# Optimization experiments

Hardware: AMD Instinct MI355X
Metric: run time of the kernel (lower is better)

The kernel has to match this reference:

```python
import jax, jax.numpy as jnp
import numpy as np

B, H, Wd, C = 8, 64, 64, 128
KH, KW = 3, 3
N = KH * KW  # kernel_n
F = 256


def _grid_offset(h, w, kh, kw):
    """Replicates the TensorLayer grid construction exactly, including the
    (2,kh,kw)->(kh*kw,2) reshape of the stacked meshgrid."""
    n = kh * kw
    initial = np.stack(np.meshgrid(np.arange(kh), np.arange(kw), indexing='ij'))  # (2,kh,kw)
    initial = initial.reshape(-1, 2).astype(np.float32)  # (n,2), faithful flattening order
    gy = np.arange(-int((kh - 1) / 2.0), h - int((kh - 1) / 2.0))
    gx = np.arange(-int((kw - 1) / 2.0), w - int((kw - 1) / 2.0))
    grid = np.stack(np.meshgrid(gy, gx, indexing='ij'), axis=-1).astype(np.float32)  # (h,w,2)
    grid = np.tile(grid[:, :, None, :], (1, 1, n, 1))  # (h,w,n,2)
    return jnp.asarray(grid + initial[None, None, :, :])  # (h,w,n,2)


def setup_inputs() -> dict:
    key = jax.random.key(0)
    k1, k2, k3 = jax.random.split(key, 3)
    x = jax.random.normal(k1, (B, H, Wd, C), dtype=jnp.float32)
    offsets = jax.random.normal(k2, (B, H, Wd, 2 * N), dtype=jnp.float32)
    W = jax.random.normal(k3, (N, C, F), dtype=jnp.float32) * 0.02  # truncated_normal(0.02) analogue
    b = jnp.zeros((F,), dtype=jnp.float32)
    return {"x": x, "offsets": offsets, "W": W, "b": b}


def reference(x, offsets, W, b):
    h, w = x.shape[1], x.shape[2]
    grid = _grid_offset(h, w, KH, KW)  # (h,w,n,2)
    coords = grid[None] + offsets.reshape(x.shape[0], h, w, N, 2)  # (b,h,w,n,2)
    cy = jnp.clip(coords[..., 0], 0.0, jnp.float32(h - 1))
    cx = jnp.clip(coords[..., 1], 0.0, jnp.float32(w - 1))
    y0 = jnp.floor(cy).astype(jnp.int32)
    y1 = jnp.ceil(cy).astype(jnp.int32)
    x0 = jnp.floor(cx).astype(jnp.int32)
    x1 = jnp.ceil(cx).astype(jnp.int32)

    bidx = jnp.arange(x.shape[0])[:, None, None, None]

    def gather(yy, xx):
        return x[bidx, yy, xx]  # (b,h,w,n,c)

    v_lt = gather(y0, x0)
    v_rb = gather(y1, x1)
    v_lb = gather(y0, x1)  # (lt_y, rb_x) as in original
    v_rt = gather(y1, x0)  # (rb_y, lt_x) as in original

    fy = (cy - y0.astype(cy.dtype))[..., None]
    fx = (cx - x0.astype(cx.dtype))[..., None]
    vals_t = v_lt + (v_rt - v_lt) * fy
    vals_b = v_lb + (v_rb - v_lb) * fy
    mapped = vals_t + (vals_b - vals_t) * fx  # (b,h,w,n,c)

    # conv3d with kernel [1,1,n,c,f] + VALID == contraction over (n,c)
    out = jnp.einsum('bhwnc,ncf->bhwf', mapped, W) + b
    return out
```

## Files before the change

kernel.cpp:

```cpp
#include <hip/hip_runtime.h>

#define HH 64
#define WW 64
#define CC 128
#define FF 256
#define NTAP 9
#define KD 1152
#define XELEMS (8 * HH * WW * CC)
#define XCVT_BLOCKS (XELEMS / (256 * 8))
#define WT_BLOCKS 144

typedef __attribute__((ext_vector_type(8))) short bf16x8;
typedef __attribute__((ext_vector_type(4))) float floatx4;

__device__ inline unsigned short f2bf(float v) {
  union { float f; unsigned u; } c; c.f = v;
  unsigned r = (c.u + 0x7FFFu + ((c.u >> 16) & 1u)) >> 16;
  return (unsigned short)r;
}
__device__ inline float bflo(unsigned u) {
  union { unsigned u; float f; } c; c.u = u << 16; return c.f;
}
__device__ inline float bfhi(unsigned u) {
  union { unsigned u; float f; } c; c.u = u & 0xFFFF0000u; return c.f;
}

__device__ inline unsigned lerp_word(unsigned u00, unsigned u10, unsigned u01, unsigned u11,
                                     float fy, float fx) {
  float v00 = bflo(u00), v10 = bflo(u10), v01 = bflo(u01), v11 = bflo(u11);
  float tx = v00 + (v10 - v00) * fy;
  float tb = v01 + (v11 - v01) * fy;
  unsigned short rlo = f2bf(tx + (tb - tx) * fx);
  v00 = bfhi(u00); v10 = bfhi(u10); v01 = bfhi(u01); v11 = bfhi(u11);
  tx = v00 + (v10 - v00) * fy;
  tb = v01 + (v11 - v01) * fy;
  unsigned short rhi = f2bf(tx + (tb - tx) * fx);
  return (unsigned)rlo | ((unsigned)rhi << 16);
}

#define IY_PACK 0x18690
#define IX_PACK 0x21894

struct ITap { int b00, b10, b01, b11; float fy, fx; };

__device__ inline ITap interp_setup(const float* __restrict__ offp, int i, int p, int nx) {
  const int n = nx >> 1;
  const float2 o2 = *(const float2*)(offp + 2 * n);
  float cy = (float)(i - 1 + ((IY_PACK >> (2 * n)) & 3)) + o2.x;
  float cx = (float)(p - 1 + ((IX_PACK >> (2 * n)) & 3)) + o2.y;
  cy = fminf(fmaxf(cy, 0.f), 63.f);
  cx = fminf(fmaxf(cx, 0.f), 63.f);
  const float fy0 = floorf(cy), fx0 = floorf(cx);
  const int y0 = (int)fy0, y1 = (int)ceilf(cy);
  const int x0 = (int)fx0, x1 = (int)ceilf(cx);
  ITap t;
  t.b00 = (y0 * WW + x0) * CC;
  t.b10 = (y1 * WW + x0) * CC;
  t.b01 = (y0 * WW + x1) * CC;
  t.b11 = (y1 * WW + x1) * CC;
  t.fy = cy - fy0;
  t.fx = cx - fx0;
  return t;
}

__global__ void prep_kernel(const float* __restrict__ X, const float* __restrict__ W,
                            unsigned short* __restrict__ Xb, unsigned short* __restrict__ Wt) {
  const int blk = blockIdx.x;
  if (blk < XCVT_BLOCKS) {
    const int t = blk * 256 + threadIdx.x;
    const float4* src = (const float4*)(X + (size_t)t * 8);
    float4 a = src[0], b2 = src[1];
    bf16x8 o;
    o[0] = (short)f2bf(a.x);  o[1] = (short)f2bf(a.y);
    o[2] = (short)f2bf(a.z);  o[3] = (short)f2bf(a.w);
    o[4] = (short)f2bf(b2.x); o[5] = (short)f2bf(b2.y);
    o[6] = (short)f2bf(b2.z); o[7] = (short)f2bf(b2.w);
    *(bf16x8*)(Xb + (size_t)t * 8) = o;
  } else {
    const int t = (blk - XCVT_BLOCKS) * 256 + threadIdx.x;
    const int f = t & 255;
    const int k0 = (t >> 8) * 8;
    unsigned short o[8];
#pragma unroll
    for (int i2 = 0; i2 < 8; ++i2)
      o[i2] = f2bf(W[(size_t)(k0 + i2) * FF + f]);
    *(uint4*)(Wt + (size_t)f * KD + k0) = *(uint4*)o;
  }
}

__global__ __launch_bounds__(256, 2) void fused_kernel(
    const unsigned short* __restrict__ Xb, const float* __restrict__ Off,
    const unsigned short* __restrict__ Wt, const float* __restrict__ bias,
    float* __restrict__ Out)
{
  __shared__ unsigned short smA[64 * 64];
  __shared__ unsigned short smB[256 * 64];

  const int blk = blockIdx.x;
  const int b   = blk & 7;
  const int i   = blk >> 3;
  const int m0  = (b * 64 + i) * 64;
  const int tid = threadIdx.x;
  const int wave = tid >> 6, lane = tid & 63;
  const int wf   = wave * 64;
  const int arow = lane & 15, aq = lane >> 4;
  const int srow = tid >> 3, sch = tid & 7;
  const int p = tid >> 2, c0 = tid & 3;

  const unsigned short* xb = Xb + (size_t)b * (HH * WW * CC);
  const float* offp = Off + ((size_t)(b * HH + i) * WW + p) * (2 * NTAP);

  floatx4 acc[4][4];
#pragma unroll
  for (int mt = 0; mt < 4; ++mt)
#pragma unroll
    for (int ft = 0; ft < 4; ++ft)
      acc[mt][ft] = (floatx4){0.f, 0.f, 0.f, 0.f};

#define STAGE_B(KT)                                                                  \
  {                                                                                  \
    _Pragma("unroll")                                                                \
    for (int q2 = 0; q2 < 8; ++q2) {                                                 \
      const int row = q2 * 32 + srow;                                                \
      const int chp = sch ^ (row & 7);                                               \
      const unsigned short* gp = Wt + (size_t)row * KD + (KT) * 64 + chp * 8;        \
      unsigned short* l = (unsigned short*)&smB[row * 64 + sch * 8];                 \
      __builtin_amdgcn_global_load_lds(                                              \
          (const __attribute__((address_space(1))) unsigned int*)gp,                 \
          (__attribute__((address_space(3))) unsigned int*)l, 16, 0, 0);             \
    }                                                                                \
  }

  {
    ITap t = interp_setup(offp, i, p, 0);
#pragma unroll
    for (int cc = 0; cc < 2; ++cc) {
      const int c = c0 + cc * 4;
      const int ch = c << 3;
      uint4 q00 = *(const uint4*)(xb + t.b00 + ch);
      uint4 q10 = *(const uint4*)(xb + t.b10 + ch);
      uint4 q01 = *(const uint4*)(xb + t.b01 + ch);
      uint4 q11 = *(const uint4*)(xb + t.b11 + ch);
      unsigned ow0 = lerp_word(q00.x, q10.x, q01.x, q11.x, t.fy, t.fx);
      unsigned ow1 = lerp_word(q00.y, q10.y, q01.y, q11.y, t.fy, t.fx);
      unsigned ow2 = lerp_word(q00.z, q10.z, q01.z, q11.z, t.fy, t.fx);
      unsigned ow3 = lerp_word(q00.w, q10.w, q01.w, q11.w, t.fy, t.fx);
      *(uint4*)&smA[p * 64 + ((c ^ (p & 7)) << 3)] = make_uint4(ow0, ow1, ow2, ow3);
    }
    STAGE_B(0)
  }
  __syncthreads();

  for (int kt = 0; kt < 18; ++kt) {
    bf16x8 afr[2][4], bfr[2][4];
#pragma unroll
    for (int ks = 0; ks < 2; ++ks) {
      const int slot = (((ks * 4 + aq) ^ (arow & 7)) << 3);
#pragma unroll
      for (int mt = 0; mt < 4; ++mt)
        afr[ks][mt] = *(const bf16x8*)&smA[(mt * 16 + arow) * 64 + slot];
#pragma unroll
      for (int ft = 0; ft < 4; ++ft)
        bfr[ks][ft] = *(const bf16x8*)&smB[(wf + ft * 16 + arow) * 64 + slot];
    }
    __syncthreads();

    const int nx = kt + 1;
    ITap t;
    uint4 g[2][4];
    if (nx < 18) {
      t = interp_setup(offp, i, p, nx);
      const int gc = (nx & 1) << 3;
#pragma unroll
      for (int cc = 0; cc < 2; ++cc) {
        const int ch = (gc + c0 + cc * 4) << 3;
        g[cc][0] = *(const uint4*)(xb + t.b00 + ch);
        g[cc][1] = *(const uint4*)(xb + t.b10 + ch);
        g[cc][2] = *(const uint4*)(xb + t.b01 + ch);
        g[cc][3] = *(const uint4*)(xb + t.b11 + ch);
      }
      STAGE_B(nx)
    }

#pragma unroll
    for (int ks = 0; ks < 2; ++ks)
#pragma unroll
      for (int mt = 0; mt < 4; ++mt)
#pragma unroll
        for (int ft = 0; ft < 4; ++ft)
          acc[mt][ft] = __builtin_amdgcn_mfma_f32_16x16x32_bf16(
              afr[ks][mt], bfr[ks][ft], acc[mt][ft], 0, 0, 0);

    if (nx < 18) {
#pragma unroll
      for (int cc = 0; cc < 2; ++cc) {
        const int c = c0 + cc * 4;
        uint4 q00 = g[cc][0], q10 = g[cc][1], q01 = g[cc][2], q11 = g[cc][3];
        unsigned ow0 = lerp_word(q00.x, q10.x, q01.x, q11.x, t.fy, t.fx);
        unsigned ow1 = lerp_word(q00.y, q10.y, q01.y, q11.y, t.fy, t.fx);
        unsigned ow2 = lerp_word(q00.z, q10.z, q01.z, q11.z, t.fy, t.fx);
        unsigned ow3 = lerp_word(q00.w, q10.w, q01.w, q11.w, t.fy, t.fx);
        *(uint4*)&smA[p * 64 + ((c ^ (p & 7)) << 3)] = make_uint4(ow0, ow1, ow2, ow3);
      }
    }
    __syncthreads();
  }
#undef STAGE_B

  float bv[4];
#pragma unroll
  for (int ft = 0; ft < 4; ++ft)
    bv[ft] = bias[wf + ft * 16 + arow];
#pragma unroll
  for (int mt = 0; mt < 4; ++mt) {
#pragma unroll
    for (int ft = 0; ft < 4; ++ft) {
      const int f = wf + ft * 16 + arow;
#pragma unroll
      for (int r = 0; r < 4; ++r) {
        const int m = m0 + mt * 16 + aq * 4 + r;
        Out[(size_t)m * FF + f] = acc[mt][ft][r] + bv[ft];
      }
    }
  }
}

extern "C" void kernel_launch(void* const* d_in, const int* in_sizes, int n_in,
                              void* d_out, int out_size, void* d_ws, size_t ws_size,
                              hipStream_t stream) {
  const float* X    = (const float*)d_in[0];
  const float* Off  = (const float*)d_in[1];
  const float* W    = (const float*)d_in[2];
  const float* bias = (const float*)d_in[3];
  float* Out = (float*)d_out;

  unsigned short* Wt = (unsigned short*)d_ws;
  unsigned short* Xb = Wt + (size_t)FF * KD;

  prep_kernel<<<XCVT_BLOCKS + WT_BLOCKS, 256, 0, stream>>>(X, W, Xb, Wt);
  fused_kernel<<<512, 256, 0, stream>>>(Xb, Off, Wt, bias, Out);
}
```

Baseline: 120.1 us.

## Use 512-thread blocks with 2x4 wave tiling and packed bf16 conversion

Doubles the fused kernel's block size to 8 waves, each computing a 32x64 output tile instead of 64x64. Each thread now gathers and interpolates one 8-channel chunk rather than two, and B staging is split across more threads. The intent is more latency hiding for the bilinear gathers and lower register pressure per thread. Separately, the manual float-to-bf16 rounding is replaced with the hardware v_cvt_pk_bf16_f32 instruction, which cuts ALU work in the lerp; in exchange each B fragment is now read from LDS by two waves.

```diff
diff --git a/kernel.cpp b/kernel.cpp
--- a/kernel.cpp
+++ b/kernel.cpp
@@ -24,18 +24,23 @@
 __device__ inline float bfhi(unsigned u) {
   union { unsigned u; float f; } c; c.u = u & 0xFFFF0000u; return c.f;
 }
+__device__ inline unsigned cvt_pk_bf16(float lo, float hi) {
+  unsigned r;
+  asm("v_cvt_pk_bf16_f32 %0, %1, %2" : "=v"(r) : "v"(lo), "v"(hi));
+  return r;
+}
 
 __device__ inline unsigned lerp_word(unsigned u00, unsigned u10, unsigned u01, unsigned u11,
                                      float fy, float fx) {
   float v00 = bflo(u00), v10 = bflo(u10), v01 = bflo(u01), v11 = bflo(u11);
   float tx = v00 + (v10 - v00) * fy;
   float tb = v01 + (v11 - v01) * fy;
-  unsigned short rlo = f2bf(tx + (tb - tx) * fx);
+  float rlo = tx + (tb - tx) * fx;
   v00 = bfhi(u00); v10 = bfhi(u10); v01 = bfhi(u01); v11 = bfhi(u11);
   tx = v00 + (v10 - v00) * fy;
   tb = v01 + (v11 - v01) * fy;
-  unsigned short rhi = f2bf(tx + (tb - tx) * fx);
-  return (unsigned)rlo | ((unsigned)rhi << 16);
+  float rhi = tx + (tb - tx) * fx;
+  return cvt_pk_bf16(rlo, rhi);
 }
 
 #define IY_PACK 0x18690
@@ -88,7 +93,7 @@
   }
 }
 
-__global__ __launch_bounds__(256, 2) void fused_kernel(
+__global__ __launch_bounds__(512, 4) void fused_kernel(
     const unsigned short* __restrict__ Xb, const float* __restrict__ Off,
     const unsigned short* __restrict__ Wt, const float* __restrict__ bias,
     float* __restrict__ Out)
@@ -102,17 +107,18 @@
   const int m0  = (b * 64 + i) * 64;
   const int tid = threadIdx.x;
   const int wave = tid >> 6, lane = tid & 63;
-  const int wf   = wave * 64;
+  const int wm   = (wave & 1) * 32;
+  const int wf   = (wave >> 1) * 64;
   const int arow = lane & 15, aq = lane >> 4;
-  const int srow = tid >> 3, sch = tid & 7;
-  const int p = tid >> 2, c0 = tid & 3;
+  const int p  = tid >> 3;
+  const int c0 = tid & 7;
 
   const unsigned short* xb = Xb + (size_t)b * (HH * WW * CC);
-  const float* offp = Off + ((size_t)(b * HH + i) * WW + p) * (2 * NTAP);
-
-  floatx4 acc[4][4];
-#pragma unroll
-  for (int mt = 0; mt < 4; ++mt)
+  const float* offp = Off + ((size_t)(b * 64 + i) * 64 + p) * (2 * NTAP);
+
+  floatx4 acc[2][4];
+#pragma unroll
+  for (int mt = 0; mt < 2; ++mt)
 #pragma unroll
     for (int ft = 0; ft < 4; ++ft)
       acc[mt][ft] = (floatx4){0.f, 0.f, 0.f, 0.f};
@@ -120,11 +126,11 @@
 #define STAGE_B(KT)                                                                  \
   {                                                                                  \
     _Pragma("unroll")                                                                \
-    for (int q2 = 0; q2 < 8; ++q2) {                                                 \
-      const int row = q2 * 32 + srow;                                                \
-      const int chp = sch ^ (row & 7);                                               \
+    for (int q2 = 0; q2 < 4; ++q2) {                                                 \
+      const int row = q2 * 64 + (tid >> 3);                                          \
+      const int chp = c0 ^ (row & 7);                                                \
       const unsigned short* gp = Wt + (size_t)row * KD + (KT) * 64 + chp * 8;        \
-      unsigned short* l = (unsigned short*)&smB[row * 64 + sch * 8];                 \
+      unsigned short* l = (unsigned short*)&smB[row * 64 + c0 * 8];                  \
       __builtin_amdgcn_global_load_lds(                                              \
           (const __attribute__((address_space(1))) unsigned int*)gp,                 \
           (__attribute__((address_space(3))) unsigned int*)l, 16, 0, 0);             \
@@ -133,32 +139,28 @@
 
   {
     ITap t = interp_setup(offp, i, p, 0);
-#pragma unroll
-    for (int cc = 0; cc < 2; ++cc) {
-      const int c = c0 + cc * 4;
-      const int ch = c << 3;
-      uint4 q00 = *(const uint4*)(xb + t.b00 + ch);
-      uint4 q10 = *(const uint4*)(xb + t.b10 + ch);
-      uint4 q01 = *(const uint4*)(xb + t.b01 + ch);
-      uint4 q11 = *(const uint4*)(xb + t.b11 + ch);
-      unsigned ow0 = lerp_word(q00.x, q10.x, q01.x, q11.x, t.fy, t.fx);
-      unsigned ow1 = lerp_word(q00.y, q10.y, q01.y, q11.y, t.fy, t.fx);
-      unsigned ow2 = lerp_word(q00.z, q10.z, q01.z, q11.z, t.fy, t.fx);
-      unsigned ow3 = lerp_word(q00.w, q10.w, q01.w, q11.w, t.fy, t.fx);
-      *(uint4*)&smA[p * 64 + ((c ^ (p & 7)) << 3)] = make_uint4(ow0, ow1, ow2, ow3);
-    }
+    const int ch = c0 * 8;
+    uint4 q00 = *(const uint4*)(xb + t.b00 + ch);
+    uint4 q10 = *(const uint4*)(xb + t.b10 + ch);
+    uint4 q01 = *(const uint4*)(xb + t.b01 + ch);
+    uint4 q11 = *(const uint4*)(xb + t.b11 + ch);
+    unsigned ow0 = lerp_word(q00.x, q10.x, q01.x, q11.x, t.fy, t.fx);
+    unsigned ow1 = lerp_word(q00.y, q10.y, q01.y, q11.y, t.fy, t.fx);
+    unsigned ow2 = lerp_word(q00.z, q10.z, q01.z, q11.z, t.fy, t.fx);
+    unsigned ow3 = lerp_word(q00.w, q10.w, q01.w, q11.w, t.fy, t.fx);
+    *(uint4*)&smA[p * 64 + ((c0 ^ (p & 7)) << 3)] = make_uint4(ow0, ow1, ow2, ow3);
     STAGE_B(0)
   }
   __syncthreads();
 
   for (int kt = 0; kt < 18; ++kt) {
-    bf16x8 afr[2][4], bfr[2][4];
+    bf16x8 afr[2][2], bfr[2][4];
 #pragma unroll
     for (int ks = 0; ks < 2; ++ks) {
       const int slot = (((ks * 4 + aq) ^ (arow & 7)) << 3);
 #pragma unroll
-      for (int mt = 0; mt < 4; ++mt)
-        afr[ks][mt] = *(const bf16x8*)&smA[(mt * 16 + arow) * 64 + slot];
+      for (int mt = 0; mt < 2; ++mt)
+        afr[ks][mt] = *(const bf16x8*)&smA[(wm + mt * 16 + arow) * 64 + slot];
 #pragma unroll
       for (int ft = 0; ft < 4; ++ft)
         bfr[ks][ft] = *(const bf16x8*)&smB[(wf + ft * 16 + arow) * 64 + slot];
@@ -167,41 +169,32 @@
 
     const int nx = kt + 1;
     ITap t;
-    uint4 g[2][4];
+    uint4 g00, g10, g01, g11;
     if (nx < 18) {
       t = interp_setup(offp, i, p, nx);
-      const int gc = (nx & 1) << 3;
-#pragma unroll
-      for (int cc = 0; cc < 2; ++cc) {
-        const int ch = (gc + c0 + cc * 4) << 3;
-        g[cc][0] = *(const uint4*)(xb + t.b00 + ch);
-        g[cc][1] = *(const uint4*)(xb + t.b10 + ch);
-        g[cc][2] = *(const uint4*)(xb + t.b01 + ch);
-        g[cc][3] = *(const uint4*)(xb + t.b11 + ch);
-      }
+      const int ch = ((nx & 1) * 8 + c0) * 8;
+      g00 = *(const uint4*)(xb + t.b00 + ch);
+      g10 = *(const uint4*)(xb + t.b10 + ch);
+      g01 = *(const uint4*)(xb + t.b01 + ch);
+      g11 = *(const uint4*)(xb + t.b11 + ch);
       STAGE_B(nx)
     }
 
 #pragma unroll
     for (int ks = 0; ks < 2; ++ks)
 #pragma unroll
-      for (int mt = 0; mt < 4; ++mt)
+      for (int mt = 0; mt < 2; ++mt)
 #pragma unroll
         for (int ft = 0; ft < 4; ++ft)
           acc[mt][ft] = __builtin_amdgcn_mfma_f32_16x16x32_bf16(
               afr[ks][mt], bfr[ks][ft], acc[mt][ft], 0, 0, 0);
 
     if (nx < 18) {
-#pragma unroll
-      for (int cc = 0; cc < 2; ++cc) {
-        const int c = c0 + cc * 4;
-        uint4 q00 = g[cc][0], q10 = g[cc][1], q01 = g[cc][2], q11 = g[cc][3];
-        unsigned ow0 = lerp_word(q00.x, q10.x, q01.x, q11.x, t.fy, t.fx);
-        unsigned ow1 = lerp_word(q00.y, q10.y, q01.y, q11.y, t.fy, t.fx);
-        unsigned ow2 = lerp_word(q00.z, q10.z, q01.z, q11.z, t.fy, t.fx);
-        unsigned ow3 = lerp_word(q00.w, q10.w, q01.w, q11.w, t.fy, t.fx);
-        *(uint4*)&smA[p * 64 + ((c ^ (p & 7)) << 3)] = make_uint4(ow0, ow1, ow2, ow3);
-      }
+      unsigned ow0 = lerp_word(g00.x, g10.x, g01.x, g11.x, t.fy, t.fx);
+      unsigned ow1 = lerp_word(g00.y, g10.y, g01.y, g11.y, t.fy, t.fx);
+      unsigned ow2 = lerp_word(g00.z, g10.z, g01.z, g11.z, t.fy, t.fx);
+      unsigned ow3 = lerp_word(g00.w, g10.w, g01.w, g11.w, t.fy, t.fx);
+      *(uint4*)&smA[p * 64 + ((c0 ^ (p & 7)) << 3)] = make_uint4(ow0, ow1, ow2, ow3);
     }
     __syncthreads();
   }
@@ -212,13 +205,13 @@
   for (int ft = 0; ft < 4; ++ft)
     bv[ft] = bias[wf + ft * 16 + arow];
 #pragma unroll
-  for (int mt = 0; mt < 4; ++mt) {
+  for (int mt = 0; mt < 2; ++mt) {
 #pragma unroll
     for (int ft = 0; ft < 4; ++ft) {
       const int f = wf + ft * 16 + arow;
 #pragma unroll
       for (int r = 0; r < 4; ++r) {
-        const int m = m0 + mt * 16 + aq * 4 + r;
+        const int m = m0 + wm + mt * 16 + aq * 4 + r;
         Out[(size_t)m * FF + f] = acc[mt][ft][r] + bv[ft];
       }
     }
@@ -238,5 +231,5 @@
   unsigned short* Xb = Wt + (size_t)FF * KD;
 
   prep_kernel<<<XCVT_BLOCKS + WT_BLOCKS, 256, 0, stream>>>(X, W, Xb, Wt);
-  fused_kernel<<<512, 256, 0, stream>>>(Xb, Off, Wt, bias, Out);
-}
+  fused_kernel<<<512, 512, 0, stream>>>(Xb, Off, Wt, bias, Out);
+}
```

New measurement: 112.6 us. 1.07x faster.

## Gather fp32 X directly, widen K-tile to a full tap, split-K across waves

Applied to the files above, without the earlier changes.

Drops the separate X-to-bf16 conversion pass, so the fused kernel gathers fp32 X and packs to bf16 with v_cvt_pk_bf16_f32. The K tile grows to one full tap (128 channels), halving the loop trip count. Block size goes to 512 threads, with two wave groups splitting K and reducing through shared memory before the store. This removes one full read/write pass over X and some barriers. In exchange the gather reads twice as many bytes, the prefetch/compute overlap is dropped, and shared memory grows to about 80KB per block.

```diff
diff --git a/kernel.cpp b/kernel.cpp
--- a/kernel.cpp
+++ b/kernel.cpp
@@ -6,8 +6,6 @@
 #define FF 256
 #define NTAP 9
 #define KD 1152
-#define XELEMS (8 * HH * WW * CC)
-#define XCVT_BLOCKS (XELEMS / (256 * 8))
 #define WT_BLOCKS 144
 
 typedef __attribute__((ext_vector_type(8))) short bf16x8;
@@ -18,24 +16,21 @@
   unsigned r = (c.u + 0x7FFFu + ((c.u >> 16) & 1u)) >> 16;
   return (unsigned short)r;
 }
-__device__ inline float bflo(unsigned u) {
-  union { unsigned u; float f; } c; c.u = u << 16; return c.f;
-}
-__device__ inline float bfhi(unsigned u) {
-  union { unsigned u; float f; } c; c.u = u & 0xFFFF0000u; return c.f;
-}
-
-__device__ inline unsigned lerp_word(unsigned u00, unsigned u10, unsigned u01, unsigned u11,
-                                     float fy, float fx) {
-  float v00 = bflo(u00), v10 = bflo(u10), v01 = bflo(u01), v11 = bflo(u11);
-  float tx = v00 + (v10 - v00) * fy;
-  float tb = v01 + (v11 - v01) * fy;
-  unsigned short rlo = f2bf(tx + (tb - tx) * fx);
-  v00 = bfhi(u00); v10 = bfhi(u10); v01 = bfhi(u01); v11 = bfhi(u11);
-  tx = v00 + (v10 - v00) * fy;
-  tb = v01 + (v11 - v01) * fy;
-  unsigned short rhi = f2bf(tx + (tb - tx) * fx);
-  return (unsigned)rlo | ((unsigned)rhi << 16);
+__device__ inline unsigned cvt_pk_bf16(float lo, float hi) {
+  unsigned r;
+  asm("v_cvt_pk_bf16_f32 %0, %1, %2" : "=v"(r) : "v"(lo), "v"(hi));
+  return r;
+}
+__device__ inline float lerp1(float v00, float v10, float v01, float v11, float fy, float fx) {
+  float t = v00 + (v10 - v00) * fy;
+  float bm = v01 + (v11 - v01) * fy;
+  return t + (bm - t) * fx;
+}
+__device__ inline unsigned lerp_pk(float A00, float A10, float A01, float A11,
+                                   float B00, float B10, float B01, float B11,
+                                   float fy, float fx) {
+  return cvt_pk_bf16(lerp1(A00, A10, A01, A11, fy, fx),
+                     lerp1(B00, B10, B01, B11, fy, fx));
 }
 
 #define IY_PACK 0x18690
@@ -43,8 +38,7 @@
 
 struct ITap { int b00, b10, b01, b11; float fy, fx; };
 
-__device__ inline ITap interp_setup(const float* __restrict__ offp, int i, int p, int nx) {
-  const int n = nx >> 1;
+__device__ inline ITap tap_setup(const float* __restrict__ offp, int i, int p, int n) {
   const float2 o2 = *(const float2*)(offp + 2 * n);
   float cy = (float)(i - 1 + ((IY_PACK >> (2 * n)) & 3)) + o2.x;
   float cx = (float)(p - 1 + ((IX_PACK >> (2 * n)) & 3)) + o2.y;
@@ -63,38 +57,47 @@
   return t;
 }
 
-__global__ void prep_kernel(const float* __restrict__ X, const float* __restrict__ W,
-                            unsigned short* __restrict__ Xb, unsigned short* __restrict__ Wt) {
-  const int blk = blockIdx.x;
-  if (blk < XCVT_BLOCKS) {
-    const int t = blk * 256 + threadIdx.x;
-    const float4* src = (const float4*)(X + (size_t)t * 8);
-    float4 a = src[0], b2 = src[1];
-    bf16x8 o;
-    o[0] = (short)f2bf(a.x);  o[1] = (short)f2bf(a.y);
-    o[2] = (short)f2bf(a.z);  o[3] = (short)f2bf(a.w);
-    o[4] = (short)f2bf(b2.x); o[5] = (short)f2bf(b2.y);
-    o[6] = (short)f2bf(b2.z); o[7] = (short)f2bf(b2.w);
-    *(bf16x8*)(Xb + (size_t)t * 8) = o;
-  } else {
-    const int t = (blk - XCVT_BLOCKS) * 256 + threadIdx.x;
-    const int f = t & 255;
-    const int k0 = (t >> 8) * 8;
-    unsigned short o[8];
-#pragma unroll
-    for (int i2 = 0; i2 < 8; ++i2)
-      o[i2] = f2bf(W[(size_t)(k0 + i2) * FF + f]);
-    *(uint4*)(Wt + (size_t)f * KD + k0) = *(uint4*)o;
-  }
-}
-
-__global__ __launch_bounds__(256, 2) void fused_kernel(
-    const unsigned short* __restrict__ Xb, const float* __restrict__ Off,
+__global__ void prep_kernel(const float* __restrict__ W, unsigned short* __restrict__ Wt) {
+  const int t = blockIdx.x * 256 + threadIdx.x;
+  const int f = t & 255;
+  const int k0 = (t >> 8) * 8;
+  unsigned short o[8];
+#pragma unroll
+  for (int i2 = 0; i2 < 8; ++i2)
+    o[i2] = f2bf(W[(size_t)(k0 + i2) * FF + f]);
+  *(uint4*)(Wt + (size_t)f * KD + k0) = *(uint4*)o;
+}
+
+__device__ inline void interp_tap(const float* __restrict__ xb, const float* __restrict__ offp,
+                                  int i, int p, int c0, int n, unsigned short* smA) {
+  ITap t = tap_setup(offp, i, p, n);
+#pragma unroll
+  for (int cc = 0; cc < 2; ++cc) {
+    const int c  = c0 + cc * 8;
+    const int ch = c * 8;
+    const float* g00 = xb + t.b00 + ch;
+    const float* g10 = xb + t.b10 + ch;
+    const float* g01 = xb + t.b01 + ch;
+    const float* g11 = xb + t.b11 + ch;
+    float4 a00 = *(const float4*)g00, e00 = *(const float4*)(g00 + 4);
+    float4 a10 = *(const float4*)g10, e10 = *(const float4*)(g10 + 4);
+    float4 a01 = *(const float4*)g01, e01 = *(const float4*)(g01 + 4);
+    float4 a11 = *(const float4*)g11, e11 = *(const float4*)(g11 + 4);
+    unsigned w0 = lerp_pk(a00.x, a10.x, a01.x, a11.x, a00.y, a10.y, a01.y, a11.y, t.fy, t.fx);
+    unsigned w1 = lerp_pk(a00.z, a10.z, a01.z, a11.z, a00.w, a10.w, a01.w, a11.w, t.fy, t.fx);
+    unsigned w2 = lerp_pk(e00.x, e10.x, e01.x, e11.x, e00.y, e10.y, e01.y, e11.y, t.fy, t.fx);
+    unsigned w3 = lerp_pk(e00.z, e10.z, e01.z, e11.z, e00.w, e10.w, e01.w, e11.w, t.fy, t.fx);
+    *(uint4*)&smA[p * 128 + ((c ^ (p & 15)) << 3)] = make_uint4(w0, w1, w2, w3);
+  }
+}
+
+__global__ __launch_bounds__(512, 4) void fused_kernel(
+    const float* __restrict__ X, const float* __restrict__ Off,
     const unsigned short* __restrict__ Wt, const float* __restrict__ bias,
     float* __restrict__ Out)
 {
-  __shared__ unsigned short smA[64 * 64];
-  __shared__ unsigned short smB[256 * 64];
+  __shared__ unsigned short smA[64 * 128];
+  __shared__ unsigned short smB[256 * 128];
 
   const int blk = blockIdx.x;
   const int b   = blk & 7;
@@ -102,12 +105,13 @@
   const int m0  = (b * 64 + i) * 64;
   const int tid = threadIdx.x;
   const int wave = tid >> 6, lane = tid & 63;
-  const int wf   = wave * 64;
+  const int kg = wave >> 2;
+  const int fg = wave & 3;
   const int arow = lane & 15, aq = lane >> 4;
-  const int srow = tid >> 3, sch = tid & 7;
-  const int p = tid >> 2, c0 = tid & 3;
-
-  const unsigned short* xb = Xb + (size_t)b * (HH * WW * CC);
+  const int p  = tid >> 3;
+  const int c0 = tid & 7;
+
+  const float* xb = X + (size_t)b * (HH * WW * CC);
   const float* offp = Off + ((size_t)(b * HH + i) * WW + p) * (2 * NTAP);
 
   floatx4 acc[4][4];
@@ -120,106 +124,79 @@
 #define STAGE_B(KT)                                                                  \
   {                                                                                  \
     _Pragma("unroll")                                                                \
-    for (int q2 = 0; q2 < 8; ++q2) {                                                 \
-      const int row = q2 * 32 + srow;                                                \
-      const int chp = sch ^ (row & 7);                                               \
-      const unsigned short* gp = Wt + (size_t)row * KD + (KT) * 64 + chp * 8;        \
-      unsigned short* l = (unsigned short*)&smB[row * 64 + sch * 8];                 \
+    for (int pass = 0; pass < 8; ++pass) {                                           \
+      const int row = pass * 32 + (tid >> 4);                                        \
+      const int kc  = tid & 15;                                                      \
+      const unsigned short* gp =                                                     \
+          Wt + (size_t)row * KD + (KT) * 128 + ((kc ^ (row & 15)) << 3);             \
+      unsigned short* l = (unsigned short*)&smB[row * 128 + kc * 8];                 \
       __builtin_amdgcn_global_load_lds(                                              \
           (const __attribute__((address_space(1))) unsigned int*)gp,                 \
           (__attribute__((address_space(3))) unsigned int*)l, 16, 0, 0);             \
     }                                                                                \
   }
 
-  {
-    ITap t = interp_setup(offp, i, p, 0);
-#pragma unroll
-    for (int cc = 0; cc < 2; ++cc) {
-      const int c = c0 + cc * 4;
-      const int ch = c << 3;
-      uint4 q00 = *(const uint4*)(xb + t.b00 + ch);
-      uint4 q10 = *(const uint4*)(xb + t.b10 + ch);
-      uint4 q01 = *(const uint4*)(xb + t.b01 + ch);
-      uint4 q11 = *(const uint4*)(xb + t.b11 + ch);
-      unsigned ow0 = lerp_word(q00.x, q10.x, q01.x, q11.x, t.fy, t.fx);
-      unsigned ow1 = lerp_word(q00.y, q10.y, q01.y, q11.y, t.fy, t.fx);
-      unsigned ow2 = lerp_word(q00.z, q10.z, q01.z, q11.z, t.fy, t.fx);
-      unsigned ow3 = lerp_word(q00.w, q10.w, q01.w, q11.w, t.fy, t.fx);
-      *(uint4*)&smA[p * 64 + ((c ^ (p & 7)) << 3)] = make_uint4(ow0, ow1, ow2, ow3);
-    }
-    STAGE_B(0)
-  }
+  STAGE_B(0)
+  interp_tap(xb, offp, i, p, c0, 0, smA);
   __syncthreads();
 
-  for (int kt = 0; kt < 18; ++kt) {
-    bf16x8 afr[2][4], bfr[2][4];
+  for (int kt = 0; kt < 9; ++kt) {
 #pragma unroll
     for (int ks = 0; ks < 2; ++ks) {
-      const int slot = (((ks * 4 + aq) ^ (arow & 7)) << 3);
+      bf16x8 afr[4], bfr[4];
+      const int slot = (((kg * 8 + ks * 4 + aq) ^ arow) << 3);
 #pragma unroll
       for (int mt = 0; mt < 4; ++mt)
-        afr[ks][mt] = *(const bf16x8*)&smA[(mt * 16 + arow) * 64 + slot];
+        afr[mt] = *(const bf16x8*)&smA[(mt * 16 + arow) * 128 + slot];
 #pragma unroll
       for (int ft = 0; ft < 4; ++ft)
-        bfr[ks][ft] = *(const bf16x8*)&smB[(wf + ft * 16 + arow) * 64 + slot];
+        bfr[ft] = *(const bf16x8*)&smB[(fg * 64 + ft * 16 + arow) * 128 + slot];
+#pragma unroll
+      for (int mt = 0; mt < 4; ++mt)
+#pragma unroll
+        for (int ft = 0; ft < 4; ++ft)
+          acc[mt][ft] = __builtin_amdgcn_mfma_f32_16x16x32_bf16(
+              afr[mt], bfr[ft], acc[mt][ft], 0, 0, 0);
     }
     __syncthreads();
 
-    const int nx = kt + 1;
-    ITap t;
-    uint4 g[2][4];
-    if (nx < 18) {
-      t = interp_setup(offp, i, p, nx);
-      const int gc = (nx & 1) << 3;
-#pragma unroll
-      for (int cc = 0; cc < 2; ++cc) {
-        const int ch = (gc + c0 + cc * 4) << 3;
-        g[cc][0] = *(const uint4*)(xb + t.b00 + ch);
-        g[cc][1] = *(const uint4*)(xb + t.b10 + ch);
-        g[cc][2] = *(const uint4*)(xb + t.b01 + ch);
-        g[cc][3] = *(const uint4*)(xb + t.b11 + ch);
+    if (kt < 8) {
+      STAGE_B(kt + 1)
+      interp_tap(xb, offp, i, p, c0, kt + 1, smA);
+      __syncthreads();
+    }
+  }
+#undef STAGE_B
+
+  float* ex = (float*)smB;
+  if (kg == 1) {
+#pragma unroll
+    for (int mt = 0; mt < 4; ++mt)
+#pragma unroll
+      for (int ft = 0; ft < 4; ++ft) {
+        const int f  = fg * 64 + ft * 16 + arow;
+        const int cm = mt * 4 + aq;
+        *(floatx4*)&ex[f * 64 + ((cm ^ arow) << 2)] = acc[mt][ft];
       }
-      STAGE_B(nx)
-    }
-
-#pragma unroll
-    for (int ks = 0; ks < 2; ++ks)
-#pragma unroll
-      for (int mt = 0; mt < 4; ++mt)
-#pragma unroll
-        for (int ft = 0; ft < 4; ++ft)
-          acc[mt][ft] = __builtin_amdgcn_mfma_f32_16x16x32_bf16(
-              afr[ks][mt], bfr[ks][ft], acc[mt][ft], 0, 0, 0);
-
-    if (nx < 18) {
-#pragma unroll
-      for (int cc = 0; cc < 2; ++cc) {
-        const int c = c0 + cc * 4;
-        uint4 q00 = g[cc][0], q10 = g[cc][1], q01 = g[cc][2], q11 = g[cc][3];
-        unsigned ow0 = lerp_word(q00.x, q10.x, q01.x, q11.x, t.fy, t.fx);
-        unsigned ow1 = lerp_word(q00.y, q10.y, q01.y, q11.y, t.fy, t.fx);
-        unsigned ow2 = lerp_word(q00.z, q10.z, q01.z, q11.z, t.fy, t.fx);
-        unsigned ow3 = lerp_word(q00.w, q10.w, q01.w, q11.w, t.fy, t.fx);
-        *(uint4*)&smA[p * 64 + ((c ^ (p & 7)) << 3)] = make_uint4(ow0, ow1, ow2, ow3);
-      }
-    }
-    __syncthreads();
-  }
-#undef STAGE_B
-
-  float bv[4];
-#pragma unroll
-  for (int ft = 0; ft < 4; ++ft)
-    bv[ft] = bias[wf + ft * 16 + arow];
-#pragma unroll
-  for (int mt = 0; mt < 4; ++mt) {
-#pragma unroll
-    for (int ft = 0; ft < 4; ++ft) {
-      const int f = wf + ft * 16 + arow;
-#pragma unroll
-      for (int r = 0; r < 4; ++r) {
-        const int m = m0 + mt * 16 + aq * 4 + r;
-        Out[(size_t)m * FF + f] = acc[mt][ft][r] + bv[ft];
+  }
+  __syncthreads();
+  if (kg == 0) {
+    float bv[4];
+#pragma unroll
+    for (int ft = 0; ft < 4; ++ft)
+      bv[ft] = bias[fg * 64 + ft * 16 + arow];
+#pragma unroll
+    for (int mt = 0; mt < 4; ++mt) {
+#pragma unroll
+      for (int ft = 0; ft < 4; ++ft) {
+        const int f  = fg * 64 + ft * 16 + arow;
+        const int cm = mt * 4 + aq;
+        floatx4 o = *(const floatx4*)&ex[f * 64 + ((cm ^ arow) << 2)];
+#pragma unroll
+        for (int r = 0; r < 4; ++r) {
+          const int m = m0 + mt * 16 + aq * 4 + r;
+          Out[(size_t)m * FF + f] = acc[mt][ft][r] + o[r] + bv[ft];
+        }
       }
     }
   }
@@ -235,8 +212,7 @@
   float* Out = (float*)d_out;
 
   unsigned short* Wt = (unsigned short*)d_ws;
-  unsigned short* Xb = Wt + (size_t)FF * KD;
-
-  prep_kernel<<<XCVT_BLOCKS + WT_BLOCKS, 256, 0, stream>>>(X, W, Xb, Wt);
-  fused_kernel<<<512, 256, 0, stream>>>(Xb, Off, Wt, bias, Out);
-}
+
+  prep_kernel<<<WT_BLOCKS, 256, 0, stream>>>(W, Wt);
+  fused_kernel<<<512, 512, 0, stream>>>(X, Off, Wt, bias, Out);
+}
```

Result: slower. 144.0 us (+20.0%).
